# Optimization experiments

Hardware: AMD Instinct MI355X
Metric: run time of the kernel (lower is better)

## Reference

```python
import jax, jax.numpy as jnp
import numpy as np

N, D, B = 500000, 128, 2048

def setup_inputs() -> dict:
    key = jax.random.key(0)
    ks = jax.random.split(key, 7)
    x = jax.random.normal(ks[0], (N, D), dtype=jnp.float32)
    batch = jnp.sort(jax.random.randint(ks[1], (N,), 0, B)).astype(jnp.int64)
    s = 1.0 / np.sqrt(D)
    Wm = jax.random.uniform(ks[2], (D, D), jnp.float32, -s, s)  # xavier-ish
    fc1_w = jax.random.uniform(ks[3], (D // 4, D), jnp.float32, -s, s)
    fc1_b = jnp.zeros((D // 4,), jnp.float32)
    fc2_w = jax.random.uniform(ks[4], (D, D // 4), jnp.float32, -1/np.sqrt(D//4), 1/np.sqrt(D//4))
    fc2_b = jnp.zeros((D,), jnp.float32)
    return {"x": x, "batch": batch, "size": B, "Wm": Wm,
            "fc1_w": fc1_w, "fc1_b": fc1_b, "fc2_w": fc2_w, "fc2_b": fc2_b}

def reference(x, batch, size, Wm, fc1_w, fc1_b, fc2_w, fc2_b):
    batch = batch.astype(jnp.int32)
    # fc: Linear -> ReLU -> Linear -> Tanh
    attention = jnp.tanh(jax.nn.relu(x @ fc1_w.T + fc1_b) @ fc2_w.T + fc2_b)
    x2 = attention * x + x  # [N, D]
    # scatter_mean over graphs
    sums = jax.ops.segment_sum(x2, batch, num_segments=size)  # [B, D]
    cnt = jax.ops.segment_sum(jnp.ones((x2.shape[0],), x2.dtype), batch, num_segments=size)
    mean = sums / jnp.maximum(cnt, 1.0)[:, None]
    transformed_global = jnp.tanh(mean @ Wm)  # [B, D]
    coefs = jax.nn.sigmoid(jnp.sum(x2 * transformed_global[batch], axis=1))  # [N]
    weighted = coefs[:, None] * x2
    return jax.ops.segment_sum(weighted, batch, num_segments=size)  # [B, D]
```

## Files before the change

kernel.cpp:

```cpp
#include <hip/hip_runtime.h>
#include <math.h>

#define D 128
#define BLOCKS_A 768
#define BLOCKS_C 1536
#define THREADS 256

typedef short s8v __attribute__((ext_vector_type(8)));
typedef float f4v __attribute__((ext_vector_type(4)));

__device__ __forceinline__ float fast_tanh(float z) {
    float e = __expf(2.f * z);
    return 1.f - 2.f / (e + 1.f);
}
__device__ __forceinline__ unsigned cvt_pk_bf16(float lo, float hi) {
    unsigned r;
    asm("v_cvt_pk_bf16_f32 %0, %1, %2" : "=v"(r) : "v"(lo), "v"(hi));
    return r;
}
__device__ __forceinline__ s8v pack8(float4 w0, float4 w1) {
    union { unsigned u[4]; s8v v; } r;
    r.u[0] = cvt_pk_bf16(w0.x, w0.y);
    r.u[1] = cvt_pk_bf16(w0.z, w0.w);
    r.u[2] = cvt_pk_bf16(w1.x, w1.y);
    r.u[3] = cvt_pk_bf16(w1.z, w1.w);
    return r.v;
}
__device__ __forceinline__ float bf2f(unsigned short h) {
    union { unsigned u; float f; } v; v.u = ((unsigned)h) << 16; return v.f;
}
__device__ __forceinline__ float bf_lo(unsigned w) {
    union { unsigned u; float f; } v; v.u = w << 16; return v.f;
}
__device__ __forceinline__ float bf_hi(unsigned w) {
    union { unsigned u; float f; } v; v.u = w & 0xffff0000u; return v.f;
}

#define RFLUSH(ACC_, SEG_, DST_)                                              \
    if ((SEG_) >= 0) {                                                        \
        _Pragma("unroll")                                                     \
        for (int t = 0; t < 8; ++t) {                                         \
            ACC_[t] += __shfl_xor(ACC_[t], 16);                               \
            ACC_[t] += __shfl_xor(ACC_[t], 32);                               \
        }                                                                     \
        _Pragma("unroll")                                                     \
        for (int t = 0; t < 8; ++t)                                           \
            if ((t >> 1) == quad)                                             \
                atomicAdd(&(DST_)[(size_t)(SEG_) * 128 + m15 + 16 * t], ACC_[t]); \
    }

#define EPI0(RG_)                                                             \
    {                                                                         \
        int r = R + quad * 4 + RG_;                                           \
        int seg = batch[r];                                                   \
        float yv[8];                                                          \
        _Pragma("unroll")                                                     \
        for (int t = 0; t < 8; ++t) {                                         \
            float xf = bf2f(xw[(quad * 4 + RG_) * 136 + m15 + 16 * t]);       \
            float z = af[t][RG_] + b2l[t];                                    \
            yv[t] = xf * (1.f + fast_tanh(z));                                \
        }                                                                     \
        union { unsigned u[4]; uint4 q; } pk;                                 \
        pk.u[0] = cvt_pk_bf16(yv[0], yv[1]);                                  \
        pk.u[1] = cvt_pk_bf16(yv[2], yv[3]);                                  \
        pk.u[2] = cvt_pk_bf16(yv[4], yv[5]);                                  \
        pk.u[3] = cvt_pk_bf16(yv[6], yv[7]);                                  \
        ((uint4*)x2s)[(size_t)b * 256 + RG_ * 64 + lane] = pk.q;              \
        if (seg == segLo) {                                                   \
            _Pragma("unroll")                                                 \
            for (int t = 0; t < 8; ++t) tl[t] += yv[t];                       \
        } else if (seg == segHi) {                                            \
            _Pragma("unroll")                                                 \
            for (int t = 0; t < 8; ++t) th[t] += yv[t];                       \
        } else {                                                              \
            _Pragma("unroll")                                                 \
            for (int t = 0; t < 8; ++t)                                       \
                atomicAdd(&sums[(size_t)seg * 128 + m15 + 16 * t], yv[t]);    \
        }                                                                     \
    }

__global__ __launch_bounds__(THREADS, 3) void phaseA(
    const float* __restrict__ x, const int* __restrict__ batch,
    const float* __restrict__ fc1_w, const float* __restrict__ fc1_b,
    const float* __restrict__ fc2_w, const float* __restrict__ fc2_b,
    float* __restrict__ sums, unsigned short* __restrict__ x2s, int N)
{
    __shared__ unsigned short xbf[4][16 * 136];
    __shared__ s8v wB1[2][4][64];
    __shared__ s8v wB2[8][64];
    __shared__ float hbuf[4][16 * 36];

    const int lane = threadIdx.x & 63;
    const int wv = threadIdx.x >> 6;
    const int m15 = lane & 15;
    const int quad = lane >> 4;

    if (wv == 0) {
        #pragma unroll
        for (int t = 0; t < 2; ++t)
            #pragma unroll
            for (int kc = 0; kc < 4; ++kc) {
                const float* p = fc1_w + (16 * t + m15) * 128 + kc * 32 + quad * 8;
                wB1[t][kc][lane] = pack8(*(const float4*)p, *(const float4*)(p + 4));
            }
        #pragma unroll
        for (int t = 0; t < 8; ++t) {
            const float* p = fc2_w + (16 * t + m15) * 32 + quad * 8;
            wB2[t][lane] = pack8(*(const float4*)p, *(const float4*)(p + 4));
        }
    }
    float b1l[2], b2l[8];
    #pragma unroll
    for (int t = 0; t < 2; ++t) b1l[t] = fc1_b[m15 + 16 * t];
    #pragma unroll
    for (int t = 0; t < 8; ++t) b2l[t] = fc2_b[m15 + 16 * t];
    __syncthreads();

    const int total16 = N >> 4;
    const int nw = BLOCKS_A * 4;
    const int gw = blockIdx.x * 4 + wv;
    const int base = total16 / nw, rem = total16 % nw;
    const int b0 = gw * base + (gw < rem ? gw : rem);
    const int b1e = b0 + base + (gw < rem ? 1 : 0);

    unsigned short* xw = xbf[wv];
    float* hw = hbuf[wv];

    float accW[8];
    #pragma unroll
    for (int t = 0; t < 8; ++t) accW[t] = 0.f;
    int curW = -1;
    const f4v z4 = {0.f, 0.f, 0.f, 0.f};

    float4 L[8];
    if (b0 < b1e) {
        const float* xp = x + (size_t)(b0 << 4) * D;
        #pragma unroll
        for (int u = 0; u < 8; ++u)
            L[u] = *(const float4*)(xp + u * 256 + lane * 4);
    }

    for (int b = b0; b < b1e; ++b) {
        const int R = b << 4;
        uint2 P[8];
        #pragma unroll
        for (int u = 0; u < 8; ++u) {
            P[u].x = cvt_pk_bf16(L[u].x, L[u].y);
            P[u].y = cvt_pk_bf16(L[u].z, L[u].w);
        }
        if (b + 1 < b1e) {
            const float* xp = x + (size_t)((b + 1) << 4) * D;
            #pragma unroll
            for (int u = 0; u < 8; ++u)
                L[u] = *(const float4*)(xp + u * 256 + lane * 4);
        }
        #pragma unroll
        for (int u = 0; u < 8; ++u) {
            int row = 2 * u + (lane >> 5);
            int col = (lane & 31) * 4;
            *(uint2*)&xw[row * 136 + col] = P[u];
        }
        s8v ax[4];
        #pragma unroll
        for (int kc = 0; kc < 4; ++kc)
            ax[kc] = *(const s8v*)&xw[m15 * 136 + kc * 32 + quad * 8];
        f4v accH[2];
        accH[0] = z4; accH[1] = z4;
        #pragma unroll
        for (int kc = 0; kc < 4; ++kc) {
            accH[0] = __builtin_amdgcn_mfma_f32_16x16x32_bf16(ax[kc], wB1[0][kc][lane], accH[0], 0, 0, 0);
            accH[1] = __builtin_amdgcn_mfma_f32_16x16x32_bf16(ax[kc], wB1[1][kc][lane], accH[1], 0, 0, 0);
        }
        #pragma unroll
        for (int t = 0; t < 2; ++t)
            #pragma unroll
            for (int rg = 0; rg < 4; ++rg) {
                float hv = fmaxf(accH[t][rg] + b1l[t], 0.f);
                hw[(quad * 4 + rg) * 36 + m15 + 16 * t] = hv;
            }
        const f4v h0 = *(const f4v*)&hw[m15 * 36 + quad * 8];
        const f4v h1 = *(const f4v*)&hw[m15 * 36 + quad * 8 + 4];
        union { unsigned u[4]; s8v v; } ahu;
        ahu.u[0] = cvt_pk_bf16(h0[0], h0[1]);
        ahu.u[1] = cvt_pk_bf16(h0[2], h0[3]);
        ahu.u[2] = cvt_pk_bf16(h1[0], h1[1]);
        ahu.u[3] = cvt_pk_bf16(h1[2], h1[3]);
        s8v ah = ahu.v;
        f4v af[8];
        #pragma unroll
        for (int t = 0; t < 8; ++t)
            af[t] = __builtin_amdgcn_mfma_f32_16x16x32_bf16(ah, wB2[t][lane], z4, 0, 0, 0);

        const int segLo = batch[R];
        const int segHi = batch[R + 15];
        float tl[8], th[8];
        #pragma unroll
        for (int t = 0; t < 8; ++t) { tl[t] = 0.f; th[t] = 0.f; }

        EPI0(0) EPI0(1) EPI0(2) EPI0(3)

        if (segLo == curW) {
            #pragma unroll
            for (int t = 0; t < 8; ++t) accW[t] += tl[t];
        } else {
            RFLUSH(accW, curW, sums)
            curW = segLo;
            #pragma unroll
            for (int t = 0; t < 8; ++t) accW[t] = tl[t];
        }
        if (segHi != segLo) {
            RFLUSH(accW, curW, sums)
            curW = segHi;
            #pragma unroll
            for (int t = 0; t < 8; ++t) accW[t] = th[t];
        }
    }
    RFLUSH(accW, curW, sums)
}

__global__ __launch_bounds__(D, 8) void phaseB(
    const float* __restrict__ sums, const int* __restrict__ batch,
    const float* __restrict__ Wm, float* __restrict__ tg, int N)
{
    int b = blockIdx.x;
    int d = threadIdx.x;
    __shared__ float m[D];
    __shared__ int bnd[2];
    if (d < 2) {
        int target = b + d;
        int lo = 0, hi = N;
        while (lo < hi) {
            int mid = (lo + hi) >> 1;
            if (batch[mid] < target) lo = mid + 1; else hi = mid;
        }
        bnd[d] = lo;
    }
    __syncthreads();
    float inv = 1.f / fmaxf((float)(bnd[1] - bnd[0]), 1.f);
    m[d] = sums[(b << 7) + d] * inv;
    __syncthreads();
    float acc = 0.f;
    #pragma unroll 8
    for (int k = 0; k < D; ++k)
        acc = fmaf(m[k], Wm[(k << 7) + d], acc);
    tg[(b << 7) + d] = fast_tanh(acc);
}

__global__ __launch_bounds__(THREADS, 4) void phaseC(
    const unsigned short* __restrict__ x2s, const int* __restrict__ batch,
    const float* __restrict__ tg, float* __restrict__ out, int N)
{
    const int lane = threadIdx.x & 63;
    const int wv = threadIdx.x >> 6;
    const int m15 = lane & 15;
    const int quad = lane >> 4;

    const int total16 = N >> 4;
    const int nw = BLOCKS_C * 4;
    const int gw = blockIdx.x * 4 + wv;
    const int base = total16 / nw, rem = total16 % nw;
    const int b0 = gw * base + (gw < rem ? gw : rem);
    const int b1e = b0 + base + (gw < rem ? 1 : 0);

    float accW[8], tgv[8];
    #pragma unroll
    for (int t = 0; t < 8; ++t) { accW[t] = 0.f; tgv[t] = 0.f; }
    int curW = -1;
    int curT = -1;

    for (int b = b0; b < b1e; ++b) {
        const int R = b << 4;
        const uint4* p = (const uint4*)x2s + (size_t)b * 256 + lane;
        uint4 C0 = p[0], C1 = p[64], C2 = p[128], C3 = p[192];
        const int segLo = batch[R];
        const int segHi = batch[R + 15];
        float tl[8], th[8];
        #pragma unroll
        for (int t = 0; t < 8; ++t) { tl[t] = 0.f; th[t] = 0.f; }

        #pragma unroll
        for (int rg = 0; rg < 4; ++rg) {
            uint4 C = rg == 0 ? C0 : rg == 1 ? C1 : rg == 2 ? C2 : C3;
            int seg = batch[R + quad * 4 + rg];
            if (seg != curT) {
                curT = seg;
                #pragma unroll
                for (int t = 0; t < 8; ++t)
                    tgv[t] = tg[(size_t)seg * 128 + m15 + 16 * t];
            }
            float xv[8];
            xv[0] = bf_lo(C.x); xv[1] = bf_hi(C.x);
            xv[2] = bf_lo(C.y); xv[3] = bf_hi(C.y);
            xv[4] = bf_lo(C.z); xv[5] = bf_hi(C.z);
            xv[6] = bf_lo(C.w); xv[7] = bf_hi(C.w);
            float dot = 0.f;
            #pragma unroll
            for (int t = 0; t < 8; ++t) dot = fmaf(xv[t], tgv[t], dot);
            dot += __shfl_xor(dot, 1);
            dot += __shfl_xor(dot, 2);
            dot += __shfl_xor(dot, 4);
            dot += __shfl_xor(dot, 8);
            float coef = 1.f / (1.f + __expf(-dot));
            if (seg == segLo) {
                #pragma unroll
                for (int t = 0; t < 8; ++t) tl[t] = fmaf(coef, xv[t], tl[t]);
            } else if (seg == segHi) {
                #pragma unroll
                for (int t = 0; t < 8; ++t) th[t] = fmaf(coef, xv[t], th[t]);
            } else {
                #pragma unroll
                for (int t = 0; t < 8; ++t)
                    atomicAdd(&out[(size_t)seg * 128 + m15 + 16 * t], coef * xv[t]);
            }
        }

        if (segLo == curW) {
            #pragma unroll
            for (int t = 0; t < 8; ++t) accW[t] += tl[t];
        } else {
            RFLUSH(accW, curW, out)
            curW = segLo;
            #pragma unroll
            for (int t = 0; t < 8; ++t) accW[t] = tl[t];
        }
        if (segHi != segLo) {
            RFLUSH(accW, curW, out)
            curW = segHi;
            #pragma unroll
            for (int t = 0; t < 8; ++t) accW[t] = th[t];
        }
    }
    RFLUSH(accW, curW, out)
}

extern "C" void kernel_launch(void* const* d_in, const int* in_sizes, int n_in,
                              void* d_out, int out_size, void* d_ws, size_t ws_size,
                              hipStream_t stream) {
    const float* x     = (const float*)d_in[0];
    const int*   batch = (const int*)d_in[1];
    const float* Wm    = (const float*)d_in[3];
    const float* fc1_w = (const float*)d_in[4];
    const float* fc1_b = (const float*)d_in[5];
    const float* fc2_w = (const float*)d_in[6];
    const float* fc2_b = (const float*)d_in[7];
    float* out = (float*)d_out;

    int N = in_sizes[0] / D;
    int B = out_size / D;

    float* sums = (float*)d_ws;
    float* tg   = sums + (size_t)B * D;
    unsigned short* x2s = (unsigned short*)(tg + (size_t)B * D);

    hipMemsetAsync(d_ws, 0, (size_t)B * D * sizeof(float), stream);
    hipMemsetAsync(d_out, 0, (size_t)out_size * sizeof(float), stream);

    phaseA<<<BLOCKS_A, THREADS, 0, stream>>>(
        x, batch, fc1_w, fc1_b, fc2_w, fc2_b, sums, x2s, N);
    phaseB<<<B, D, 0, stream>>>(sums, batch, Wm, tg, N);
    phaseC<<<BLOCKS_C, THREADS, 0, stream>>>(x2s, batch, tg, out, N);
}
```

Baseline: 438.9 us.

## Fuse global transform into weighting pass with one wave per segment

```diff
diff --git a/kernel.cpp b/kernel.cpp
--- a/kernel.cpp
+++ b/kernel.cpp
@@ -3,7 +3,6 @@
 
 #define D 128
 #define BLOCKS_A 768
-#define BLOCKS_C 1536
 #define THREADS 256
 
 typedef short s8v __attribute__((ext_vector_type(8)));
@@ -218,81 +217,76 @@
     RFLUSH(accW, curW, sums)
 }
 
-__global__ __launch_bounds__(D, 8) void phaseB(
-    const float* __restrict__ sums, const int* __restrict__ batch,
-    const float* __restrict__ Wm, float* __restrict__ tg, int N)
+__global__ __launch_bounds__(THREADS, 4) void phaseCB(
+    const unsigned short* __restrict__ x2s, const int* __restrict__ batch,
+    const float* __restrict__ sums, const float* __restrict__ Wm,
+    float* __restrict__ out, int N, int B)
 {
-    int b = blockIdx.x;
-    int d = threadIdx.x;
-    __shared__ float m[D];
-    __shared__ int bnd[2];
-    if (d < 2) {
-        int target = b + d;
-        int lo = 0, hi = N;
-        while (lo < hi) {
-            int mid = (lo + hi) >> 1;
-            if (batch[mid] < target) lo = mid + 1; else hi = mid;
-        }
-        bnd[d] = lo;
-    }
-    __syncthreads();
-    float inv = 1.f / fmaxf((float)(bnd[1] - bnd[0]), 1.f);
-    m[d] = sums[(b << 7) + d] * inv;
-    __syncthreads();
-    float acc = 0.f;
-    #pragma unroll 8
-    for (int k = 0; k < D; ++k)
-        acc = fmaf(m[k], Wm[(k << 7) + d], acc);
-    tg[(b << 7) + d] = fast_tanh(acc);
-}
-
-__global__ __launch_bounds__(THREADS, 4) void phaseC(
-    const unsigned short* __restrict__ x2s, const int* __restrict__ batch,
-    const float* __restrict__ tg, float* __restrict__ out, int N)
-{
+    __shared__ float lmean[4][D];
+    __shared__ float ltg[4][D];
+
     const int lane = threadIdx.x & 63;
     const int wv = threadIdx.x >> 6;
     const int m15 = lane & 15;
     const int quad = lane >> 4;
 
-    const int total16 = N >> 4;
-    const int nw = BLOCKS_C * 4;
-    const int gw = blockIdx.x * 4 + wv;
-    const int base = total16 / nw, rem = total16 % nw;
-    const int b0 = gw * base + (gw < rem ? gw : rem);
-    const int b1e = b0 + base + (gw < rem ? 1 : 0);
-
-    float accW[8], tgv[8];
-    #pragma unroll
-    for (int t = 0; t < 8; ++t) { accW[t] = 0.f; tgv[t] = 0.f; }
-    int curW = -1;
-    int curT = -1;
-
-    for (int b = b0; b < b1e; ++b) {
+    const int s = blockIdx.x * 4 + wv;
+    if (s >= B) return;
+
+    int lo = 0, hi = N;
+    while (lo < hi) { int mid = (lo + hi) >> 1; if (batch[mid] < s) lo = mid + 1; else hi = mid; }
+    int lo1 = lo, hi1 = N;
+    while (lo1 < hi1) { int mid = (lo1 + hi1) >> 1; if (batch[mid] < s + 1) lo1 = mid + 1; else hi1 = mid; }
+    const int rlo = lo, rhi = lo1;
+
+    float invc = 1.f / fmaxf((float)(rhi - rlo), 1.f);
+    lmean[wv][lane]      = sums[(size_t)s * 128 + lane] * invc;
+    lmean[wv][lane + 64] = sums[(size_t)s * 128 + lane + 64] * invc;
+    float a0 = 0.f, a1 = 0.f;
+    #pragma unroll 8
+    for (int k = 0; k < D; ++k) {
+        float mk = lmean[wv][k];
+        a0 = fmaf(mk, Wm[(size_t)k * 128 + lane], a0);
+        a1 = fmaf(mk, Wm[(size_t)k * 128 + lane + 64], a1);
+    }
+    ltg[wv][lane]      = fast_tanh(a0);
+    ltg[wv][lane + 64] = fast_tanh(a1);
+    float tgv[8];
+    #pragma unroll
+    for (int t = 0; t < 8; ++t) tgv[t] = ltg[wv][m15 + 16 * t];
+
+    float acc[8];
+    #pragma unroll
+    for (int t = 0; t < 8; ++t) acc[t] = 0.f;
+
+    const int tb0 = rlo >> 4;
+    const int tb1 = (rhi + 15) >> 4;
+
+    uint4 P[4];
+    if (tb0 < tb1) {
+        const uint4* p = (const uint4*)x2s + (size_t)tb0 * 256 + lane;
+        #pragma unroll
+        for (int rg = 0; rg < 4; ++rg) P[rg] = p[rg * 64];
+    }
+
+    for (int b = tb0; b < tb1; ++b) {
+        uint4 C[4];
+        #pragma unroll
+        for (int rg = 0; rg < 4; ++rg) C[rg] = P[rg];
+        if (b + 1 < tb1) {
+            const uint4* p = (const uint4*)x2s + (size_t)(b + 1) * 256 + lane;
+            #pragma unroll
+            for (int rg = 0; rg < 4; ++rg) P[rg] = p[rg * 64];
+        }
         const int R = b << 4;
-        const uint4* p = (const uint4*)x2s + (size_t)b * 256 + lane;
-        uint4 C0 = p[0], C1 = p[64], C2 = p[128], C3 = p[192];
-        const int segLo = batch[R];
-        const int segHi = batch[R + 15];
-        float tl[8], th[8];
-        #pragma unroll
-        for (int t = 0; t < 8; ++t) { tl[t] = 0.f; th[t] = 0.f; }
-
         #pragma unroll
         for (int rg = 0; rg < 4; ++rg) {
-            uint4 C = rg == 0 ? C0 : rg == 1 ? C1 : rg == 2 ? C2 : C3;
-            int seg = batch[R + quad * 4 + rg];
-            if (seg != curT) {
-                curT = seg;
-                #pragma unroll
-                for (int t = 0; t < 8; ++t)
-                    tgv[t] = tg[(size_t)seg * 128 + m15 + 16 * t];
-            }
+            const int row = R + quad * 4 + rg;
             float xv[8];
-            xv[0] = bf_lo(C.x); xv[1] = bf_hi(C.x);
-            xv[2] = bf_lo(C.y); xv[3] = bf_hi(C.y);
-            xv[4] = bf_lo(C.z); xv[5] = bf_hi(C.z);
-            xv[6] = bf_lo(C.w); xv[7] = bf_hi(C.w);
+            xv[0] = bf_lo(C[rg].x); xv[1] = bf_hi(C[rg].x);
+            xv[2] = bf_lo(C[rg].y); xv[3] = bf_hi(C[rg].y);
+            xv[4] = bf_lo(C[rg].z); xv[5] = bf_hi(C[rg].z);
+            xv[6] = bf_lo(C[rg].w); xv[7] = bf_hi(C[rg].w);
             float dot = 0.f;
             #pragma unroll
             for (int t = 0; t < 8; ++t) dot = fmaf(xv[t], tgv[t], dot);
@@ -301,36 +295,22 @@
             dot += __shfl_xor(dot, 4);
             dot += __shfl_xor(dot, 8);
             float coef = 1.f / (1.f + __expf(-dot));
-            if (seg == segLo) {
+            if (row >= rlo && row < rhi) {
                 #pragma unroll
-                for (int t = 0; t < 8; ++t) tl[t] = fmaf(coef, xv[t], tl[t]);
-            } else if (seg == segHi) {
-                #pragma unroll
-                for (int t = 0; t < 8; ++t) th[t] = fmaf(coef, xv[t], th[t]);
-            } else {
-                #pragma unroll
-                for (int t = 0; t < 8; ++t)
-                    atomicAdd(&out[(size_t)seg * 128 + m15 + 16 * t], coef * xv[t]);
+                for (int t = 0; t < 8; ++t) acc[t] = fmaf(coef, xv[t], acc[t]);
             }
         }
-
-        if (segLo == curW) {
-            #pragma unroll
-            for (int t = 0; t < 8; ++t) accW[t] += tl[t];
-        } else {
-            RFLUSH(accW, curW, out)
-            curW = segLo;
-            #pragma unroll
-            for (int t = 0; t < 8; ++t) accW[t] = tl[t];
-        }
-        if (segHi != segLo) {
-            RFLUSH(accW, curW, out)
-            curW = segHi;
-            #pragma unroll
-            for (int t = 0; t < 8; ++t) accW[t] = th[t];
-        }
-    }
-    RFLUSH(accW, curW, out)
+    }
+
+    #pragma unroll
+    for (int t = 0; t < 8; ++t) {
+        acc[t] += __shfl_xor(acc[t], 16);
+        acc[t] += __shfl_xor(acc[t], 32);
+    }
+    #pragma unroll
+    for (int t = 0; t < 8; ++t)
+        if ((t >> 1) == quad)
+            out[(size_t)s * 128 + m15 + 16 * t] = acc[t];
 }
 
 extern "C" void kernel_launch(void* const* d_in, const int* in_sizes, int n_in,
@@ -349,14 +329,12 @@
     int B = out_size / D;
 
     float* sums = (float*)d_ws;
-    float* tg   = sums + (size_t)B * D;
-    unsigned short* x2s = (unsigned short*)(tg + (size_t)B * D);
+    unsigned short* x2s = (unsigned short*)(sums + (size_t)B * D);
 
     hipMemsetAsync(d_ws, 0, (size_t)B * D * sizeof(float), stream);
-    hipMemsetAsync(d_out, 0, (size_t)out_size * sizeof(float), stream);
 
     phaseA<<<BLOCKS_A, THREADS, 0, stream>>>(
         x, batch, fc1_w, fc1_b, fc2_w, fc2_b, sums, x2s, N);
-    phaseB<<<B, D, 0, stream>>>(sums, batch, Wm, tg, N);
-    phaseC<<<BLOCKS_C, THREADS, 0, stream>>>(x2s, batch, tg, out, N);
-}
+    phaseCB<<<(B + 3) / 4, THREADS, 0, stream>>>(
+        x2s, batch, sums, Wm, out, N, B);
+}
```

Result: faster. 425.9 us (-2.9%).
